# Performance work log

Hardware: AMD Instinct MI355X
Metric: run time of the kernel (lower is better)

## Reference

```python
import jax, jax.numpy as jnp
import numpy as np

N = 50000        # num nodes
E = 800000       # num edges (before self loops)
IN = 256         # in_channels
H = 4            # heads
C = 32           # out_channels per head
NEG_SLOPE = 0.2


def _glorot(key, shape):
    fan = shape[-2] * (shape[-1] if len(shape) > 2 else 1) + shape[-1]
    # PyG glorot: uniform(-s, s) with s = sqrt(6 / (fan_in + fan_out))
    s = float(np.sqrt(6.0 / (shape[-2] + shape[-1])))
    return jax.random.uniform(key, shape, jnp.float32, -s, s)


def setup_inputs() -> dict:
    key = jax.random.key(0)
    k1, k2, k3, k4, k5 = jax.random.split(key, 5)
    x = jax.random.normal(k1, (N, IN), jnp.float32)
    src = jax.random.randint(k2, (E,), 0, N)
    dst = jax.random.randint(k3, (E,), 0, N)
    # guarantee no self loops (module removes them then re-adds exactly N loops)
    dst = jnp.where(dst == src, (dst + 1) % N, dst)
    edge_index = jnp.stack([src, dst]).astype(jnp.int32)
    weight = _glorot(k4, (IN, H * C))
    att = _glorot(k5, (1, H, 2 * C))
    bias = jnp.zeros((H * C,), jnp.float32)
    return {"x": x, "weight": weight, "att": att, "bias": bias,
            "edge_index": edge_index}


def reference(x, weight, att, bias, edge_index):
    n = x.shape[0]
    # linear projection -> [N, H, C]
    h = (x @ weight).reshape(n, H, C)
    # add self loops (input edge_index has none)
    loops = jnp.arange(n, dtype=edge_index.dtype)
    ei = jnp.concatenate([edge_index, jnp.stack([loops, loops])], axis=1)
    src, dst = ei[0], ei[1]          # flow source_to_target: j=src(row 0), i=dst(row 1)
    x_j = h[src]                     # [E', H, C] source features
    x_i = h[dst]                     # [E', H, C] target features
    wl = att[:, :, :C]               # applied to x_i (first half of concat)
    wr = att[:, :, C:]               # applied to x_j
    alpha = (x_i * wl).sum(-1) + (x_j * wr).sum(-1)   # [E', H]
    alpha = jax.nn.leaky_relu(alpha, NEG_SLOPE)
    # NOTE: module normalizes softmax over edge_index[0] (src) segments
    seg = src
    amax = jax.ops.segment_max(alpha, seg, num_segments=n)
    alpha = jnp.exp(alpha - amax[seg])
    denom = jax.ops.segment_sum(alpha, seg, num_segments=n)
    alpha = alpha / (denom[seg] + 1e-16)
    # weighted messages, aggregated at edge_index[i] = edge_index[1] (dst)
    msg = x_j * alpha[:, :, None]                     # [E', H, C]
    out = jax.ops.segment_sum(msg, dst, num_segments=n)  # [N, H, C]
    return out.reshape(n, H * C) + bias
```

## Files before the change

kernel.cpp:

```cpp
#include <hip/hip_runtime.h>
#include <hip/hip_fp16.h>
#include <math.h>


#define NH 4
#define CH 32
#define HC 128
#define IND 256
#define NEG_SLOPE 0.2f
#define CSH 8
#define NCB_MAX 256
#define CHUNK 4096

typedef __attribute__((ext_vector_type(8))) short bf16x8;
typedef __attribute__((ext_vector_type(16))) float f32x16;

__device__ __forceinline__ unsigned short f2bf(float f) {
    unsigned int u = __float_as_uint(f);
    unsigned int r = (u + 0x7FFFu + ((u >> 16) & 1u)) >> 16;
    return (unsigned short)r;
}
__device__ __forceinline__ float bf2f(unsigned short s) {
    return __uint_as_float(((unsigned int)s) << 16);
}

__global__ __launch_bounds__(256) void k_init0(int* __restrict__ histS,
                                               int* __restrict__ histD, int ncb) {
    int t = threadIdx.x;
    if (t < ncb) { histS[t] = 0; histD[t] = 0; }
}

__global__ __launch_bounds__(256) void k_wprep(const float* __restrict__ W,
                                               unsigned short* __restrict__ WT_bf) {
    int t = blockIdx.x * 256 + threadIdx.x;
    if (t >= IND * HC) return;
    int c = t >> 8;
    int k = t & 255;
    WT_bf[t] = f2bf(W[k * HC + c]);
}

__global__ __launch_bounds__(256) void k_gemm_mfma(const float* __restrict__ x,
                                                   const unsigned short* __restrict__ WT_bf,
                                                   const float* __restrict__ att,
                                                   unsigned short* __restrict__ h_bf,
                                                   float* __restrict__ al,
                                                   float* __restrict__ ar, int N) {
    __shared__ float cs[128 * 129];
    unsigned short* wsT = (unsigned short*)cs;

    const int tid  = threadIdx.x;
    const int row0 = blockIdx.x * 128;
    const int wave = tid >> 6;
    const int lane = tid & 63;
    const int n32  = lane & 31;
    const int half = lane >> 5;

    {
        int c  = tid >> 1;
        int kh = (tid & 1) * 128;
        const unsigned short* src = WT_bf + c * IND + kh;
        unsigned short* dst = wsT + c * 258 + kh;
#pragma unroll
        for (int j = 0; j < 128; j += 8)
            *(int4*)(dst + j) = *(const int4*)(src + j);
    }
    __syncthreads();

    const int row   = row0 + wave * 32 + n32;
    const bool valid = row < N;
    const float* xrow = x + (size_t)row * IND + half * 8;

    f32x16 acc[4];
#pragma unroll
    for (int t = 0; t < 4; t++)
#pragma unroll
        for (int r = 0; r < 16; r++) acc[t][r] = 0.0f;

#pragma unroll 4
    for (int s = 0; s < 16; s++) {
        float4 v0 = make_float4(0.f, 0.f, 0.f, 0.f);
        float4 v1 = v0;
        if (valid) {
            v0 = *(const float4*)(xrow + s * 16);
            v1 = *(const float4*)(xrow + s * 16 + 4);
        }
        bf16x8 a;
        a[0] = (short)f2bf(v0.x); a[1] = (short)f2bf(v0.y);
        a[2] = (short)f2bf(v0.z); a[3] = (short)f2bf(v0.w);
        a[4] = (short)f2bf(v1.x); a[5] = (short)f2bf(v1.y);
        a[6] = (short)f2bf(v1.z); a[7] = (short)f2bf(v1.w);
#pragma unroll
        for (int t = 0; t < 4; t++) {
            bf16x8 b = *(const bf16x8*)(wsT + (t * 32 + n32) * 258 + s * 16 + half * 8);
            acc[t] = __builtin_amdgcn_mfma_f32_32x32x16_bf16(a, b, acc[t], 0, 0, 0);
        }
    }
    __syncthreads();

#pragma unroll
    for (int t = 0; t < 4; t++)
#pragma unroll
        for (int r = 0; r < 16; r++) {
            int rl = wave * 32 + (r & 3) + 8 * (r >> 2) + 4 * half;
            cs[rl * 129 + t * 32 + n32] = acc[t][r];
        }
    __syncthreads();

    const int rl   = tid >> 1;
    const int chf  = tid & 1;
    const int orow = row0 + rl;
    if (orow < N) {
        const float* cr = cs + rl * 129 + chf * 64;
        unsigned short* hp = h_bf + (size_t)orow * HC + chf * 64;
#pragma unroll
        for (int c = 0; c < 64; c += 8) {
            ushort4 o0, o1;
            o0.x = f2bf(cr[c]);     o0.y = f2bf(cr[c + 1]);
            o0.z = f2bf(cr[c + 2]); o0.w = f2bf(cr[c + 3]);
            o1.x = f2bf(cr[c + 4]); o1.y = f2bf(cr[c + 5]);
            o1.z = f2bf(cr[c + 6]); o1.w = f2bf(cr[c + 7]);
            *(ushort4*)(hp + c) = o0;
            *(ushort4*)(hp + c + 4) = o1;
        }
        const int h0 = 2 * chf, h1 = 2 * chf + 1;
        const float* w0 = att + h0 * (2 * CH);
        const float* w1 = att + h1 * (2 * CH);
        float sl0 = 0.f, sr0 = 0.f, sl1 = 0.f, sr1 = 0.f;
#pragma unroll
        for (int c = 0; c < CH; c++) {
            float v0 = cr[c];
            float v1 = cr[CH + c];
            sl0 += v0 * w0[c];  sr0 += v0 * w0[CH + c];
            sl1 += v1 * w1[c];  sr1 += v1 * w1[CH + c];
        }
        al[orow * NH + h0] = sl0;  al[orow * NH + h1] = sl1;
        ar[orow * NH + h0] = sr0;  ar[orow * NH + h1] = sr1;
    }
}

__global__ __launch_bounds__(256) void k_hist(const int* __restrict__ ei,
                                              int* __restrict__ histS,
                                              int* __restrict__ histD,
                                              int E, int NE, int ncb) {
    __shared__ int hs[NCB_MAX], hd[NCB_MAX];
    hs[threadIdx.x] = 0; hd[threadIdx.x] = 0;
    __syncthreads();
    for (int t = blockIdx.x * 256 + threadIdx.x; t < NE; t += gridDim.x * 256) {
        int src, dst;
        if (t < E) { src = ei[t]; dst = ei[E + t]; }
        else       { src = dst = t - E; }
        atomicAdd(&hs[src >> CSH], 1);
        atomicAdd(&hd[dst >> CSH], 1);
    }
    __syncthreads();
    int i = threadIdx.x;
    if (i < ncb) {
        if (hs[i]) atomicAdd(&histS[i], hs[i]);
        if (hd[i]) atomicAdd(&histD[i], hd[i]);
    }
}

__global__ __launch_bounds__(256) void k_scanC(const int* __restrict__ histS,
                                               const int* __restrict__ histD,
                                               int* __restrict__ baseS,
                                               int* __restrict__ baseD,
                                               int* __restrict__ curS,
                                               int* __restrict__ curD,
                                               int* __restrict__ rowptrS,
                                               int* __restrict__ rowptrD,
                                               int ncb, int NE, int N) {
    __shared__ int sc[256];
    int tid = threadIdx.x;
    int v = (tid < ncb) ? histS[tid] : 0;
    sc[tid] = v;
    __syncthreads();
    for (int o = 1; o < 256; o <<= 1) {
        int t = (tid >= o) ? sc[tid - o] : 0;
        __syncthreads();
        sc[tid] += t;
        __syncthreads();
    }
    if (tid < ncb) { baseS[tid] = sc[tid] - v; curS[tid] = sc[tid] - v; }
    if (tid == 0) { baseS[ncb] = sc[255]; rowptrS[N] = NE; }
    __syncthreads();
    v = (tid < ncb) ? histD[tid] : 0;
    sc[tid] = v;
    __syncthreads();
    for (int o = 1; o < 256; o <<= 1) {
        int t = (tid >= o) ? sc[tid - o] : 0;
        __syncthreads();
        sc[tid] += t;
        __syncthreads();
    }
    if (tid < ncb) { baseD[tid] = sc[tid] - v; curD[tid] = sc[tid] - v; }
    if (tid == 0) { baseD[ncb] = sc[255]; rowptrD[N] = NE; }
}

__global__ __launch_bounds__(256) void k_scatterC(const int* __restrict__ ei,
                                                  int* __restrict__ gcurS,
                                                  int* __restrict__ gcurD,
                                                  unsigned int* __restrict__ recS,
                                                  unsigned int* __restrict__ recD,
                                                  int E, int NE, int ncb) {
    __shared__ unsigned int srt[CHUNK];
    __shared__ int cnt[NCB_MAX], off[NCB_MAX], cur[NCB_MAX], gpos[NCB_MAX], sc[256];
    const int tid = threadIdx.x;
    const int t0  = blockIdx.x * CHUNK;
    const int m   = min(CHUNK, NE - t0);

    unsigned int myrec[CHUNK / 256];
    int nmy = 0;
    for (int i = tid; i < m; i += 256) {
        int t = t0 + i;
        int src, dst;
        if (t < E) { src = ei[t]; dst = ei[E + t]; }
        else       { src = dst = t - E; }
        myrec[nmy++] = (unsigned int)src | ((unsigned int)dst << 16);
    }

    for (int side = 0; side < 2; side++) {
        cnt[tid] = 0;
        __syncthreads();
        int mybkt[CHUNK / 256];
        for (int k = 0; k < nmy; k++) {
            unsigned int r = myrec[k];
            int node = side ? (int)(r >> 16) : (int)(r & 0xFFFFu);
            mybkt[k] = node >> CSH;
            atomicAdd(&cnt[mybkt[k]], 1);
        }
        __syncthreads();
        int v = cnt[tid];
        sc[tid] = v;
        __syncthreads();
        for (int o = 1; o < 256; o <<= 1) {
            int t = (tid >= o) ? sc[tid - o] : 0;
            __syncthreads();
            sc[tid] += t;
            __syncthreads();
        }
        off[tid] = sc[tid] - v;
        cur[tid] = sc[tid] - v;
        __syncthreads();
        for (int k = 0; k < nmy; k++) {
            int p = atomicAdd(&cur[mybkt[k]], 1);
            srt[p] = myrec[k];
        }
        __syncthreads();
        int* gcur = side ? gcurD : gcurS;
        if (tid < ncb) {
            int c = cnt[tid];
            gpos[tid] = c ? atomicAdd(&gcur[tid], c) : 0;
        }
        __syncthreads();
        unsigned int* recX = side ? recD : recS;
        for (int i = tid; i < m; i += 256) {
            unsigned int r = srt[i];
            int node = side ? (int)(r >> 16) : (int)(r & 0xFFFFu);
            int cb = node >> CSH;
            recX[gpos[cb] + (i - off[cb])] = r;
        }
        __syncthreads();
    }
}

__global__ __launch_bounds__(256) void k_rebin(const unsigned int* __restrict__ recS,
                                               const unsigned int* __restrict__ recD,
                                               const int* __restrict__ baseS,
                                               const int* __restrict__ baseD,
                                               unsigned short* __restrict__ adjS,
                                               unsigned short* __restrict__ adjD,
                                               int* __restrict__ rowptrS,
                                               int* __restrict__ rowptrD,
                                               int ncb, int N) {
    __shared__ int cnt[256], cur[256], sc[256];
    const int tid  = threadIdx.x;
    const int side = (blockIdx.x >= ncb) ? 1 : 0;
    const int cb   = side ? blockIdx.x - ncb : blockIdx.x;
    const unsigned int* rec = side ? recD : recS;
    const int* base = side ? baseD : baseS;
    const int b0 = base[cb], b1 = base[cb + 1];
    const int tot_rec = b1 - b0;

    cnt[tid] = 0;
    __syncthreads();
    for (int i = tid; i < tot_rec; i += 256) {
        unsigned int r = rec[b0 + i];
        int node = side ? (int)(r >> 16) : (int)(r & 0xFFFFu);
        atomicAdd(&cnt[node & 255], 1);
    }
    __syncthreads();
    int v = cnt[tid];
    sc[tid] = v;
    __syncthreads();
    for (int o = 1; o < 256; o <<= 1) {
        int t = (tid >= o) ? sc[tid - o] : 0;
        __syncthreads();
        sc[tid] += t;
        __syncthreads();
    }
    int ex = sc[tid] - v;
    int node_g = (cb << CSH) + tid;
    int* rowptr = side ? rowptrD : rowptrS;
    if (node_g < N) rowptr[node_g] = b0 + ex;
    cur[tid] = ex;
    __syncthreads();
    unsigned short* adj = side ? adjD : adjS;
    for (int i = tid; i < tot_rec; i += 256) {
        unsigned int r = rec[b0 + i];
        int node = side ? (int)(r >> 16) : (int)(r & 0xFFFFu);
        unsigned short other = side ? (unsigned short)(r & 0xFFFFu)
                                    : (unsigned short)(r >> 16);
        int p = atomicAdd(&cur[node & 255], 1);
        adj[b0 + p] = other;
    }
}

__global__ __launch_bounds__(256) void k_denom(const int* __restrict__ rowptrS,
                                               const unsigned short* __restrict__ adjS,
                                               const float* __restrict__ al,
                                               const float* __restrict__ ar,
                                               float* __restrict__ arw, int N) {
    int n = blockIdx.x * 256 + threadIdx.x;
    if (n >= N) return;
    int beg = rowptrS[n], end = rowptrS[n + 1];
    float4 arv = *(const float4*)(ar + n * NH);
    float s0 = 0.f, s1 = 0.f, s2 = 0.f, s3 = 0.f;
    int i = beg;
    for (; i + 2 <= end; i += 2) {
        int d0 = adjS[i], d1 = adjS[i + 1];
        float4 av0 = *(const float4*)(al + d0 * NH);
        float4 av1 = *(const float4*)(al + d1 * NH);
        float a0 = av0.x + arv.x, a1 = av0.y + arv.y;
        float a2 = av0.z + arv.z, a3 = av0.w + arv.w;
        float c0 = av1.x + arv.x, c1 = av1.y + arv.y;
        float c2 = av1.z + arv.z, c3 = av1.w + arv.w;
        a0 = (a0 > 0.f) ? a0 : NEG_SLOPE * a0;
        a1 = (a1 > 0.f) ? a1 : NEG_SLOPE * a1;
        a2 = (a2 > 0.f) ? a2 : NEG_SLOPE * a2;
        a3 = (a3 > 0.f) ? a3 : NEG_SLOPE * a3;
        c0 = (c0 > 0.f) ? c0 : NEG_SLOPE * c0;
        c1 = (c1 > 0.f) ? c1 : NEG_SLOPE * c1;
        c2 = (c2 > 0.f) ? c2 : NEG_SLOPE * c2;
        c3 = (c3 > 0.f) ? c3 : NEG_SLOPE * c3;
        s0 += __expf(a0) + __expf(c0);
        s1 += __expf(a1) + __expf(c1);
        s2 += __expf(a2) + __expf(c2);
        s3 += __expf(a3) + __expf(c3);
    }
    if (i < end) {
        int d0 = adjS[i];
        float4 av = *(const float4*)(al + d0 * NH);
        float a0 = av.x + arv.x, a1 = av.y + arv.y;
        float a2 = av.z + arv.z, a3 = av.w + arv.w;
        a0 = (a0 > 0.f) ? a0 : NEG_SLOPE * a0;
        a1 = (a1 > 0.f) ? a1 : NEG_SLOPE * a1;
        a2 = (a2 > 0.f) ? a2 : NEG_SLOPE * a2;
        a3 = (a3 > 0.f) ? a3 : NEG_SLOPE * a3;
        s0 += __expf(a0); s1 += __expf(a1);
        s2 += __expf(a2); s3 += __expf(a3);
    }
    float r0 = 1.0f / (s0 + 1e-16f);
    float r1 = 1.0f / (s1 + 1e-16f);
    float r2 = 1.0f / (s2 + 1e-16f);
    float r3 = 1.0f / (s3 + 1e-16f);
    float4 p0 = make_float4(arv.x, r0, arv.y, r1);
    float4 p1 = make_float4(arv.z, r2, arv.w, r3);
    *(float4*)(arw + (size_t)n * 8)     = p0;
    *(float4*)(arw + (size_t)n * 8 + 4) = p1;
}

__global__ __launch_bounds__(256) void k_agg(const int* __restrict__ rowptrD,
                                             const unsigned short* __restrict__ adjD,
                                             const float* __restrict__ al,
                                             const float* __restrict__ arw,
                                             const unsigned short* __restrict__ h_bf,
                                             const float* __restrict__ bias,
                                             float* __restrict__ out, int N) {
    const int g = threadIdx.x >> 5;
    const int n = blockIdx.x * 8 + g;
    if (n >= N) return;
    const int l  = threadIdx.x & 31;
    const int c0 = l * 4;
    const int hh = l >> 3;
    const int beg = rowptrD[n], end = rowptrD[n + 1];
    const float alv = al[n * NH + hh];

    float a0 = 0.f, a1 = 0.f, a2 = 0.f, a3 = 0.f;

    for (int base = beg; base < end; base += 32) {
        int idx = base + l;
        int av  = (idx < end) ? (int)adjD[idx] : 0;
        int cnt = min(32, end - base);
        int e = 0;
        for (; e + 4 <= cnt; e += 4) {
            int s0 = __shfl(av, e,     32);
            int s1 = __shfl(av, e + 1, 32);
            int s2 = __shfl(av, e + 2, 32);
            int s3 = __shfl(av, e + 3, 32);
            ushort4 u0 = *(const ushort4*)(h_bf + (size_t)s0 * HC + c0);
            ushort4 u1 = *(const ushort4*)(h_bf + (size_t)s1 * HC + c0);
            ushort4 u2 = *(const ushort4*)(h_bf + (size_t)s2 * HC + c0);
            ushort4 u3 = *(const ushort4*)(h_bf + (size_t)s3 * HC + c0);
            float2 p0 = *(const float2*)(arw + (size_t)s0 * 8 + hh * 2);
            float2 p1 = *(const float2*)(arw + (size_t)s1 * 8 + hh * 2);
            float2 p2 = *(const float2*)(arw + (size_t)s2 * 8 + hh * 2);
            float2 p3 = *(const float2*)(arw + (size_t)s3 * 8 + hh * 2);
            float t0 = alv + p0.x; t0 = (t0 > 0.f) ? t0 : NEG_SLOPE * t0;
            float t1 = alv + p1.x; t1 = (t1 > 0.f) ? t1 : NEG_SLOPE * t1;
            float t2 = alv + p2.x; t2 = (t2 > 0.f) ? t2 : NEG_SLOPE * t2;
            float t3 = alv + p3.x; t3 = (t3 > 0.f) ? t3 : NEG_SLOPE * t3;
            float w0 = __expf(t0) * p0.y;
            float w1 = __expf(t1) * p1.y;
            float w2 = __expf(t2) * p2.y;
            float w3 = __expf(t3) * p3.y;
            a0 += bf2f(u0.x) * w0; a1 += bf2f(u0.y) * w0;
            a2 += bf2f(u0.z) * w0; a3 += bf2f(u0.w) * w0;
            a0 += bf2f(u1.x) * w1; a1 += bf2f(u1.y) * w1;
            a2 += bf2f(u1.z) * w1; a3 += bf2f(u1.w) * w1;
            a0 += bf2f(u2.x) * w2; a1 += bf2f(u2.y) * w2;
            a2 += bf2f(u2.z) * w2; a3 += bf2f(u2.w) * w2;
            a0 += bf2f(u3.x) * w3; a1 += bf2f(u3.y) * w3;
            a2 += bf2f(u3.z) * w3; a3 += bf2f(u3.w) * w3;
        }
        for (; e < cnt; e++) {
            int s0 = __shfl(av, e, 32);
            ushort4 u0 = *(const ushort4*)(h_bf + (size_t)s0 * HC + c0);
            float2 p0 = *(const float2*)(arw + (size_t)s0 * 8 + hh * 2);
            float t0 = alv + p0.x; t0 = (t0 > 0.f) ? t0 : NEG_SLOPE * t0;
            float w0 = __expf(t0) * p0.y;
            a0 += bf2f(u0.x) * w0; a1 += bf2f(u0.y) * w0;
            a2 += bf2f(u0.z) * w0; a3 += bf2f(u0.w) * w0;
        }
    }
    float4 b4 = *(const float4*)(bias + c0);
    *(float4*)(out + (size_t)n * HC + c0) =
        make_float4(a0 + b4.x, a1 + b4.y, a2 + b4.z, a3 + b4.w);
}

extern "C" void kernel_launch(void* const* d_in, const int* in_sizes, int n_in,
                              void* d_out, int out_size, void* d_ws, size_t ws_size,
                              hipStream_t stream) {
    const float* x    = (const float*)d_in[0];
    const float* W    = (const float*)d_in[1];
    const float* att  = (const float*)d_in[2];
    const float* bias = (const float*)d_in[3];
    const int*   ei   = (const int*)d_in[4];

    const int N  = in_sizes[0] / IND;
    const int E  = in_sizes[4] / 2;
    const int NE = E + N;
    const int ncb = (N + (1 << CSH) - 1) >> CSH;
    float* out = (float*)d_out;
    const int nodeTot = N * NH;

    unsigned short* h_bf  = (unsigned short*)d_ws;
    unsigned short* WT_bf = h_bf + (size_t)N * HC;
    float* al      = (float*)(WT_bf + IND * HC);
    float* ar      = al + nodeTot;
    float* rdenom  = ar + nodeTot;
    unsigned int* recS = (unsigned int*)(rdenom + nodeTot);
    unsigned int* recD = recS + NE;
    unsigned short* adjS = (unsigned short*)(recD + NE);
    unsigned short* adjD = adjS + NE;
    unsigned short* wD   = adjD + NE + (NE & 1);
    int* rowptrS = (int*)(wD + (size_t)NE * NH);
    int* rowptrD = rowptrS + (N + 2);
    int* histS   = rowptrD + (N + 2);
    int* histD   = histS + NCB_MAX;
    int* baseS   = histD + NCB_MAX;
    int* baseD   = baseS + (NCB_MAX + 1);
    int* curS    = baseD + (NCB_MAX + 1);
    int* curD    = curS + NCB_MAX;
    float* arw = (float*)((((uintptr_t)(curD + NCB_MAX)) + 255) & ~(uintptr_t)255);

    k_init0<<<1, 256, 0, stream>>>(histS, histD, ncb);
    k_wprep<<<(IND * HC + 255) / 256, 256, 0, stream>>>(W, WT_bf);
    k_gemm_mfma<<<(N + 127) / 128, 256, 0, stream>>>(x, WT_bf, att, h_bf, al, ar, N);
    k_hist<<<256, 256, 0, stream>>>(ei, histS, histD, E, NE, ncb);
    k_scanC<<<1, 256, 0, stream>>>(histS, histD, baseS, baseD, curS, curD,
                                   rowptrS, rowptrD, ncb, NE, N);
    k_scatterC<<<(NE + CHUNK - 1) / CHUNK, 256, 0, stream>>>(ei, curS, curD,
                                                             recS, recD, E, NE, ncb);
    k_rebin<<<2 * ncb, 256, 0, stream>>>(recS, recD, baseS, baseD, adjS, adjD,
                                         rowptrS, rowptrD, ncb, N);
    k_denom<<<(N + 255) / 256, 256, 0, stream>>>(rowptrS, adjS, al, ar, arw, N);
    k_agg<<<(N + 7) / 8, 256, 0, stream>>>(rowptrD, adjD, al, arw, h_bf, bias, out, N);
}
```

Baseline: 225.7 us.

## Compute softmax denominators with per-edge atomics, drop source-side CSR build

Replaces the source-grouped CSR construction (histogram, scan, scatter, rebin for src) and its per-node denominator kernel with a single edge-parallel kernel. That kernel computes exp(leaky_relu) per edge and atomically adds it into per-source sums. The reciprocal packing into arw moves into the histogram kernel, and the zeroing of sums and histD moves into the weight prep kernel, which removes a launch. This halves the sorting work but adds about 3.2M float atomics to global memory, and the summation order becomes nondeterministic.

```diff
diff --git a/kernel.cpp b/kernel.cpp
--- a/kernel.cpp
+++ b/kernel.cpp
@@ -24,19 +24,19 @@
     return __uint_as_float(((unsigned int)s) << 16);
 }
 
-__global__ __launch_bounds__(256) void k_init0(int* __restrict__ histS,
-                                               int* __restrict__ histD, int ncb) {
-    int t = threadIdx.x;
-    if (t < ncb) { histS[t] = 0; histD[t] = 0; }
-}
-
 __global__ __launch_bounds__(256) void k_wprep(const float* __restrict__ W,
-                                               unsigned short* __restrict__ WT_bf) {
+                                               unsigned short* __restrict__ WT_bf,
+                                               int* __restrict__ histD,
+                                               float* __restrict__ sums,
+                                               int nodeTot) {
     int t = blockIdx.x * 256 + threadIdx.x;
-    if (t >= IND * HC) return;
-    int c = t >> 8;
-    int k = t & 255;
-    WT_bf[t] = f2bf(W[k * HC + c]);
+    if (blockIdx.x == 0) histD[threadIdx.x] = 0;
+    for (int i = t; i < nodeTot; i += gridDim.x * 256) sums[i] = 0.f;
+    if (t < IND * HC) {
+        int c = t >> 8;
+        int k = t & 255;
+        WT_bf[t] = f2bf(W[k * HC + c]);
+    }
 }
 
 __global__ __launch_bounds__(256) void k_gemm_mfma(const float* __restrict__ x,
@@ -138,40 +138,69 @@
     }
 }
 
+__global__ __launch_bounds__(256) void k_denomE(const int* __restrict__ ei,
+                                                const float* __restrict__ al,
+                                                const float* __restrict__ ar,
+                                                float* __restrict__ sums,
+                                                int E, int NE) {
+    int t = blockIdx.x * 256 + threadIdx.x;
+    if (t >= NE) return;
+    int src, dst;
+    if (t < E) { src = ei[t]; dst = ei[E + t]; }
+    else       { src = dst = t - E; }
+    float4 alv = *(const float4*)(al + (size_t)dst * NH);
+    float4 arv = *(const float4*)(ar + (size_t)src * NH);
+    float a0 = alv.x + arv.x, a1 = alv.y + arv.y;
+    float a2 = alv.z + arv.z, a3 = alv.w + arv.w;
+    a0 = (a0 > 0.f) ? a0 : NEG_SLOPE * a0;
+    a1 = (a1 > 0.f) ? a1 : NEG_SLOPE * a1;
+    a2 = (a2 > 0.f) ? a2 : NEG_SLOPE * a2;
+    a3 = (a3 > 0.f) ? a3 : NEG_SLOPE * a3;
+    float* sp = sums + (size_t)src * NH;
+    atomicAdd(sp + 0, __expf(a0));
+    atomicAdd(sp + 1, __expf(a1));
+    atomicAdd(sp + 2, __expf(a2));
+    atomicAdd(sp + 3, __expf(a3));
+}
+
 __global__ __launch_bounds__(256) void k_hist(const int* __restrict__ ei,
-                                              int* __restrict__ histS,
                                               int* __restrict__ histD,
-                                              int E, int NE, int ncb) {
-    __shared__ int hs[NCB_MAX], hd[NCB_MAX];
-    hs[threadIdx.x] = 0; hd[threadIdx.x] = 0;
+                                              const float* __restrict__ ar,
+                                              const float* __restrict__ sums,
+                                              float* __restrict__ arw,
+                                              int E, int NE, int ncb, int N) {
+    __shared__ int hd[NCB_MAX];
+    for (int n = blockIdx.x * 256 + threadIdx.x; n < N; n += gridDim.x * 256) {
+        float4 arv = *(const float4*)(ar + (size_t)n * NH);
+        float4 sv  = *(const float4*)(sums + (size_t)n * NH);
+        float4 p0 = make_float4(arv.x, 1.0f / (sv.x + 1e-16f),
+                                arv.y, 1.0f / (sv.y + 1e-16f));
+        float4 p1 = make_float4(arv.z, 1.0f / (sv.z + 1e-16f),
+                                arv.w, 1.0f / (sv.w + 1e-16f));
+        *(float4*)(arw + (size_t)n * 8)     = p0;
+        *(float4*)(arw + (size_t)n * 8 + 4) = p1;
+    }
+    hd[threadIdx.x] = 0;
     __syncthreads();
     for (int t = blockIdx.x * 256 + threadIdx.x; t < NE; t += gridDim.x * 256) {
-        int src, dst;
-        if (t < E) { src = ei[t]; dst = ei[E + t]; }
-        else       { src = dst = t - E; }
-        atomicAdd(&hs[src >> CSH], 1);
+        int dst;
+        if (t < E) dst = ei[E + t];
+        else       dst = t - E;
         atomicAdd(&hd[dst >> CSH], 1);
     }
     __syncthreads();
     int i = threadIdx.x;
-    if (i < ncb) {
-        if (hs[i]) atomicAdd(&histS[i], hs[i]);
-        if (hd[i]) atomicAdd(&histD[i], hd[i]);
-    }
-}
-
-__global__ __launch_bounds__(256) void k_scanC(const int* __restrict__ histS,
-                                               const int* __restrict__ histD,
-                                               int* __restrict__ baseS,
+    if (i < ncb && hd[i]) atomicAdd(&histD[i], hd[i]);
+}
+
+__global__ __launch_bounds__(256) void k_scanC(const int* __restrict__ histD,
                                                int* __restrict__ baseD,
-                                               int* __restrict__ curS,
                                                int* __restrict__ curD,
-                                               int* __restrict__ rowptrS,
                                                int* __restrict__ rowptrD,
                                                int ncb, int NE, int N) {
     __shared__ int sc[256];
     int tid = threadIdx.x;
-    int v = (tid < ncb) ? histS[tid] : 0;
+    int v = (tid < ncb) ? histD[tid] : 0;
     sc[tid] = v;
     __syncthreads();
     for (int o = 1; o < 256; o <<= 1) {
@@ -180,26 +209,12 @@
         sc[tid] += t;
         __syncthreads();
     }
-    if (tid < ncb) { baseS[tid] = sc[tid] - v; curS[tid] = sc[tid] - v; }
-    if (tid == 0) { baseS[ncb] = sc[255]; rowptrS[N] = NE; }
-    __syncthreads();
-    v = (tid < ncb) ? histD[tid] : 0;
-    sc[tid] = v;
-    __syncthreads();
-    for (int o = 1; o < 256; o <<= 1) {
-        int t = (tid >= o) ? sc[tid - o] : 0;
-        __syncthreads();
-        sc[tid] += t;
-        __syncthreads();
-    }
     if (tid < ncb) { baseD[tid] = sc[tid] - v; curD[tid] = sc[tid] - v; }
     if (tid == 0) { baseD[ncb] = sc[255]; rowptrD[N] = NE; }
 }
 
 __global__ __launch_bounds__(256) void k_scatterC(const int* __restrict__ ei,
-                                                  int* __restrict__ gcurS,
                                                   int* __restrict__ gcurD,
-                                                  unsigned int* __restrict__ recS,
                                                   unsigned int* __restrict__ recD,
                                                   int E, int NE, int ncb) {
     __shared__ unsigned int srt[CHUNK];
@@ -209,84 +224,66 @@
     const int m   = min(CHUNK, NE - t0);
 
     unsigned int myrec[CHUNK / 256];
+    int mybkt[CHUNK / 256];
     int nmy = 0;
+    cnt[tid] = 0;
+    __syncthreads();
     for (int i = tid; i < m; i += 256) {
         int t = t0 + i;
         int src, dst;
         if (t < E) { src = ei[t]; dst = ei[E + t]; }
         else       { src = dst = t - E; }
-        myrec[nmy++] = (unsigned int)src | ((unsigned int)dst << 16);
-    }
-
-    for (int side = 0; side < 2; side++) {
-        cnt[tid] = 0;
-        __syncthreads();
-        int mybkt[CHUNK / 256];
-        for (int k = 0; k < nmy; k++) {
-            unsigned int r = myrec[k];
-            int node = side ? (int)(r >> 16) : (int)(r & 0xFFFFu);
-            mybkt[k] = node >> CSH;
-            atomicAdd(&cnt[mybkt[k]], 1);
-        }
-        __syncthreads();
-        int v = cnt[tid];
-        sc[tid] = v;
-        __syncthreads();
-        for (int o = 1; o < 256; o <<= 1) {
-            int t = (tid >= o) ? sc[tid - o] : 0;
-            __syncthreads();
-            sc[tid] += t;
-            __syncthreads();
-        }
-        off[tid] = sc[tid] - v;
-        cur[tid] = sc[tid] - v;
-        __syncthreads();
-        for (int k = 0; k < nmy; k++) {
-            int p = atomicAdd(&cur[mybkt[k]], 1);
-            srt[p] = myrec[k];
-        }
-        __syncthreads();
-        int* gcur = side ? gcurD : gcurS;
-        if (tid < ncb) {
-            int c = cnt[tid];
-            gpos[tid] = c ? atomicAdd(&gcur[tid], c) : 0;
-        }
-        __syncthreads();
-        unsigned int* recX = side ? recD : recS;
-        for (int i = tid; i < m; i += 256) {
-            unsigned int r = srt[i];
-            int node = side ? (int)(r >> 16) : (int)(r & 0xFFFFu);
-            int cb = node >> CSH;
-            recX[gpos[cb] + (i - off[cb])] = r;
-        }
-        __syncthreads();
-    }
-}
-
-__global__ __launch_bounds__(256) void k_rebin(const unsigned int* __restrict__ recS,
-                                               const unsigned int* __restrict__ recD,
-                                               const int* __restrict__ baseS,
+        myrec[nmy] = (unsigned int)src | ((unsigned int)dst << 16);
+        mybkt[nmy] = dst >> CSH;
+        atomicAdd(&cnt[mybkt[nmy]], 1);
+        nmy++;
+    }
+    __syncthreads();
+    int v = cnt[tid];
+    sc[tid] = v;
+    __syncthreads();
+    for (int o = 1; o < 256; o <<= 1) {
+        int t = (tid >= o) ? sc[tid - o] : 0;
+        __syncthreads();
+        sc[tid] += t;
+        __syncthreads();
+    }
+    off[tid] = sc[tid] - v;
+    cur[tid] = sc[tid] - v;
+    __syncthreads();
+    for (int k = 0; k < nmy; k++) {
+        int p = atomicAdd(&cur[mybkt[k]], 1);
+        srt[p] = myrec[k];
+    }
+    __syncthreads();
+    if (tid < ncb) {
+        int c = cnt[tid];
+        gpos[tid] = c ? atomicAdd(&gcurD[tid], c) : 0;
+    }
+    __syncthreads();
+    for (int i = tid; i < m; i += 256) {
+        unsigned int r = srt[i];
+        int cb = (int)(r >> 16) >> CSH;
+        recD[gpos[cb] + (i - off[cb])] = r;
+    }
+}
+
+__global__ __launch_bounds__(256) void k_rebin(const unsigned int* __restrict__ recD,
                                                const int* __restrict__ baseD,
-                                               unsigned short* __restrict__ adjS,
                                                unsigned short* __restrict__ adjD,
-                                               int* __restrict__ rowptrS,
                                                int* __restrict__ rowptrD,
                                                int ncb, int N) {
     __shared__ int cnt[256], cur[256], sc[256];
-    const int tid  = threadIdx.x;
-    const int side = (blockIdx.x >= ncb) ? 1 : 0;
-    const int cb   = side ? blockIdx.x - ncb : blockIdx.x;
-    const unsigned int* rec = side ? recD : recS;
-    const int* base = side ? baseD : baseS;
-    const int b0 = base[cb], b1 = base[cb + 1];
+    const int tid = threadIdx.x;
+    const int cb  = blockIdx.x;
+    const int b0 = baseD[cb], b1 = baseD[cb + 1];
     const int tot_rec = b1 - b0;
 
     cnt[tid] = 0;
     __syncthreads();
     for (int i = tid; i < tot_rec; i += 256) {
-        unsigned int r = rec[b0 + i];
-        int node = side ? (int)(r >> 16) : (int)(r & 0xFFFFu);
-        atomicAdd(&cnt[node & 255], 1);
+        unsigned int r = recD[b0 + i];
+        atomicAdd(&cnt[(r >> 16) & 255], 1);
     }
     __syncthreads();
     int v = cnt[tid];
@@ -300,73 +297,15 @@
     }
     int ex = sc[tid] - v;
     int node_g = (cb << CSH) + tid;
-    int* rowptr = side ? rowptrD : rowptrS;
-    if (node_g < N) rowptr[node_g] = b0 + ex;
+    if (node_g < N) rowptrD[node_g] = b0 + ex;
     cur[tid] = ex;
     __syncthreads();
-    unsigned short* adj = side ? adjD : adjS;
     for (int i = tid; i < tot_rec; i += 256) {
-        unsigned int r = rec[b0 + i];
-        int node = side ? (int)(r >> 16) : (int)(r & 0xFFFFu);
-        unsigned short other = side ? (unsigned short)(r & 0xFFFFu)
-                                    : (unsigned short)(r >> 16);
-        int p = atomicAdd(&cur[node & 255], 1);
-        adj[b0 + p] = other;
-    }
-}
-
-__global__ __launch_bounds__(256) void k_denom(const int* __restrict__ rowptrS,
-                                               const unsigned short* __restrict__ adjS,
-                                               const float* __restrict__ al,
-                                               const float* __restrict__ ar,
-                                               float* __restrict__ arw, int N) {
-    int n = blockIdx.x * 256 + threadIdx.x;
-    if (n >= N) return;
-    int beg = rowptrS[n], end = rowptrS[n + 1];
-    float4 arv = *(const float4*)(ar + n * NH);
-    float s0 = 0.f, s1 = 0.f, s2 = 0.f, s3 = 0.f;
-    int i = beg;
-    for (; i + 2 <= end; i += 2) {
-        int d0 = adjS[i], d1 = adjS[i + 1];
-        float4 av0 = *(const float4*)(al + d0 * NH);
-        float4 av1 = *(const float4*)(al + d1 * NH);
-        float a0 = av0.x + arv.x, a1 = av0.y + arv.y;
-        float a2 = av0.z + arv.z, a3 = av0.w + arv.w;
-        float c0 = av1.x + arv.x, c1 = av1.y + arv.y;
-        float c2 = av1.z + arv.z, c3 = av1.w + arv.w;
-        a0 = (a0 > 0.f) ? a0 : NEG_SLOPE * a0;
-        a1 = (a1 > 0.f) ? a1 : NEG_SLOPE * a1;
-        a2 = (a2 > 0.f) ? a2 : NEG_SLOPE * a2;
-        a3 = (a3 > 0.f) ? a3 : NEG_SLOPE * a3;
-        c0 = (c0 > 0.f) ? c0 : NEG_SLOPE * c0;
-        c1 = (c1 > 0.f) ? c1 : NEG_SLOPE * c1;
-        c2 = (c2 > 0.f) ? c2 : NEG_SLOPE * c2;
-        c3 = (c3 > 0.f) ? c3 : NEG_SLOPE * c3;
-        s0 += __expf(a0) + __expf(c0);
-        s1 += __expf(a1) + __expf(c1);
-        s2 += __expf(a2) + __expf(c2);
-        s3 += __expf(a3) + __expf(c3);
-    }
-    if (i < end) {
-        int d0 = adjS[i];
-        float4 av = *(const float4*)(al + d0 * NH);
-        float a0 = av.x + arv.x, a1 = av.y + arv.y;
-        float a2 = av.z + arv.z, a3 = av.w + arv.w;
-        a0 = (a0 > 0.f) ? a0 : NEG_SLOPE * a0;
-        a1 = (a1 > 0.f) ? a1 : NEG_SLOPE * a1;
-        a2 = (a2 > 0.f) ? a2 : NEG_SLOPE * a2;
-        a3 = (a3 > 0.f) ? a3 : NEG_SLOPE * a3;
-        s0 += __expf(a0); s1 += __expf(a1);
-        s2 += __expf(a2); s3 += __expf(a3);
-    }
-    float r0 = 1.0f / (s0 + 1e-16f);
-    float r1 = 1.0f / (s1 + 1e-16f);
-    float r2 = 1.0f / (s2 + 1e-16f);
-    float r3 = 1.0f / (s3 + 1e-16f);
-    float4 p0 = make_float4(arv.x, r0, arv.y, r1);
-    float4 p1 = make_float4(arv.z, r2, arv.w, r3);
-    *(float4*)(arw + (size_t)n * 8)     = p0;
-    *(float4*)(arw + (size_t)n * 8 + 4) = p1;
+        unsigned int r = recD[b0 + i];
+        int node = (int)(r >> 16) & 255;
+        int p = atomicAdd(&cur[node], 1);
+        adjD[b0 + p] = (unsigned short)(r & 0xFFFFu);
+    }
 }
 
 __global__ __launch_bounds__(256) void k_agg(const int* __restrict__ rowptrD,
@@ -455,34 +394,23 @@
 
     unsigned short* h_bf  = (unsigned short*)d_ws;
     unsigned short* WT_bf = h_bf + (size_t)N * HC;
-    float* al      = (float*)(WT_bf + IND * HC);
-    float* ar      = al + nodeTot;
-    float* rdenom  = ar + nodeTot;
-    unsigned int* recS = (unsigned int*)(rdenom + nodeTot);
-    unsigned int* recD = recS + NE;
-    unsigned short* adjS = (unsigned short*)(recD + NE);
-    unsigned short* adjD = adjS + NE;
-    unsigned short* wD   = adjD + NE + (NE & 1);
-    int* rowptrS = (int*)(wD + (size_t)NE * NH);
-    int* rowptrD = rowptrS + (N + 2);
-    int* histS   = rowptrD + (N + 2);
-    int* histD   = histS + NCB_MAX;
-    int* baseS   = histD + NCB_MAX;
-    int* baseD   = baseS + (NCB_MAX + 1);
-    int* curS    = baseD + (NCB_MAX + 1);
-    int* curD    = curS + NCB_MAX;
-    float* arw = (float*)((((uintptr_t)(curD + NCB_MAX)) + 255) & ~(uintptr_t)255);
-
-    k_init0<<<1, 256, 0, stream>>>(histS, histD, ncb);
-    k_wprep<<<(IND * HC + 255) / 256, 256, 0, stream>>>(W, WT_bf);
+    float* al   = (float*)(WT_bf + IND * HC);
+    float* ar   = al + nodeTot;
+    float* sums = ar + nodeTot;
+    float* arw  = sums + nodeTot;
+    unsigned int* recD = (unsigned int*)(arw + (size_t)N * 8);
+    unsigned short* adjD = (unsigned short*)(recD + NE);
+    int* rowptrD = (int*)(adjD + NE + (NE & 1));
+    int* histD   = rowptrD + (N + 2);
+    int* baseD   = histD + NCB_MAX;
+    int* curD    = baseD + (NCB_MAX + 1);
+
+    k_wprep<<<(IND * HC + 255) / 256, 256, 0, stream>>>(W, WT_bf, histD, sums, nodeTot);
     k_gemm_mfma<<<(N + 127) / 128, 256, 0, stream>>>(x, WT_bf, att, h_bf, al, ar, N);
-    k_hist<<<256, 256, 0, stream>>>(ei, histS, histD, E, NE, ncb);
-    k_scanC<<<1, 256, 0, stream>>>(histS, histD, baseS, baseD, curS, curD,
-                                   rowptrS, rowptrD, ncb, NE, N);
-    k_scatterC<<<(NE + CHUNK - 1) / CHUNK, 256, 0, stream>>>(ei, curS, curD,
-                                                             recS, recD, E, NE, ncb);
-    k_rebin<<<2 * ncb, 256, 0, stream>>>(recS, recD, baseS, baseD, adjS, adjD,
-                                         rowptrS, rowptrD, ncb, N);
-    k_denom<<<(N + 255) / 256, 256, 0, stream>>>(rowptrS, adjS, al, ar, arw, N);
+    k_denomE<<<(NE + 255) / 256, 256, 0, stream>>>(ei, al, ar, sums, E, NE);
+    k_hist<<<256, 256, 0, stream>>>(ei, histD, ar, sums, arw, E, NE, ncb, N);
+    k_scanC<<<1, 256, 0, stream>>>(histD, baseD, curD, rowptrD, ncb, NE, N);
+    k_scatterC<<<(NE + CHUNK - 1) / CHUNK, 256, 0, stream>>>(ei, curD, recD, E, NE, ncb);
+    k_rebin<<<ncb, 256, 0, stream>>>(recD, baseD, adjD, rowptrD, ncb, N);
     k_agg<<<(N + 7) / 8, 256, 0, stream>>>(rowptrD, adjD, al, arw, h_bf, bias, out, N);
 }
```

After: 366.5 us. 62.4% more time.
